# Optimization experiments

Hardware: AMD Instinct MI355X
Metric: run time of the kernel (lower is better)

The kernel has to match this reference:

```python
import jax, jax.numpy as jnp
import numpy as np

B, S, D = 2, 1024, 1024
H, KVH, HD = 16, 4, 64  # query heads, kv heads, head_dim
EPS = 1e-5
SCALE = float(np.sqrt(HD))  # note: scale uses original head_dim, not concat dim


def rmsnorm(x, g):
    return x * jax.lax.rsqrt(jnp.mean(x * x, axis=-1, keepdims=True) + EPS) * g


def rope(x, cos, sin):
    # x: [B,S,h,HD]; cos/sin: [S, HD//2]; pairs are consecutive (view_as_complex layout)
    xr = x.reshape(*x.shape[:-1], HD // 2, 2)
    x0, x1 = xr[..., 0], xr[..., 1]
    c = cos[None, :, None, :]
    s = sin[None, :, None, :]
    o0 = x0 * c - x1 * s
    o1 = x0 * s + x1 * c
    return jnp.stack([o0, o1], axis=-1).reshape(x.shape)


def context_build(x, W, gq, gk):
    comb = x @ W.T  # [B,S, H*HD + 2*KVH*HD]
    q, k, v = jnp.split(comb, [H * HD, H * HD + KVH * HD], axis=-1)
    q = rmsnorm(q, gq).reshape(B, S, H, HD)
    k = rmsnorm(k, gk).reshape(B, S, KVH, HD)
    v = v.reshape(B, S, KVH, HD)
    return q, k, v


def setup_inputs() -> dict:
    key = jax.random.key(0)
    ks = jax.random.split(key, 12)
    total = H * HD + 2 * KVH * HD  # 1536
    pos = jnp.arange(S, dtype=jnp.float32)
    theta = 10000.0 ** (-jnp.arange(0, HD, 2, dtype=jnp.float32) / HD)  # [HD//2]
    ang = pos[:, None] * theta[None, :]  # [S, HD//2]
    sc = 0.02
    return {
        "local_c": jax.random.normal(ks[0], (B, S, D), jnp.float32),
        "global_c": jax.random.normal(ks[1], (B, S, D), jnp.float32),
        "freqs_cos": jnp.cos(ang),
        "freqs_sin": jnp.sin(ang),
        "W_lc": jax.random.normal(ks[2], (total, D), jnp.float32) * sc,
        "W_gc": jax.random.normal(ks[3], (total, D), jnp.float32) * sc,
        "g_q_lc": jnp.ones((H * HD,), jnp.float32),
        "g_k_lc": jnp.ones((KVH * HD,), jnp.float32),
        "g_q_gc": jnp.ones((H * HD,), jnp.float32),
        "g_k_gc": jnp.ones((KVH * HD,), jnp.float32),
        "W_local": jax.random.normal(ks[4], (H * HD, 2 * H * HD), jnp.float32) * sc,
        "b_local": jnp.zeros((H * HD,), jnp.float32),
        "g_lc_out": jnp.ones((H * HD,), jnp.float32),
        "W_global": jax.random.normal(ks[5], (H * HD, 2 * H * HD), jnp.float32) * sc,
        "b_global": jnp.zeros((H * HD,), jnp.float32),
        "g_gc_out": jnp.ones((H * HD,), jnp.float32),
    }


def reference(local_c, global_c, freqs_cos, freqs_sin, W_lc, W_gc,
              g_q_lc, g_k_lc, g_q_gc, g_k_gc,
              W_local, b_local, g_lc_out, W_global, b_global, g_gc_out):
    q_lc, k_lc, v_lc = context_build(local_c, W_lc, g_q_lc, g_k_lc)
    q_gc, k_gc, v_gc = context_build(global_c, W_gc, g_q_gc, g_k_gc)

    q_lc = rope(q_lc, freqs_cos, freqs_sin)
    k_lc = rope(k_lc, freqs_cos, freqs_sin)
    q_gc = rope(q_gc, freqs_cos, freqs_sin)
    k_gc = rope(k_gc, freqs_cos, freqs_sin)

    # concat local+global along head_dim -> per-head dim 2*HD
    q = jnp.concatenate([q_lc, q_gc], axis=-1)  # [B,S,H,2HD]
    k = jnp.concatenate([k_lc, k_gc], axis=-1)  # [B,S,KVH,2HD]
    v = jnp.concatenate([v_lc, v_gc], axis=-1)

    n_rep = H // KVH
    k = jnp.repeat(k, n_rep, axis=2)  # [B,S,H,2HD] (GQA repeat_kv)
    v = jnp.repeat(v, n_rep, axis=2)

    scores = jnp.einsum("bqhd,bkhd->bhqk", q, k) / SCALE  # [B,H,S,S]
    attn = jax.nn.softmax(scores, axis=-1)
    out = jnp.einsum("bhqk,bkhd->bqhd", attn, v).reshape(B, S, H * 2 * HD)

    x_lc = rmsnorm(out @ W_local.T + b_local, g_lc_out)
    x_gc = rmsnorm(out @ W_global.T + b_global, g_gc_out)
    return (x_lc, x_gc)
```

## Files before the change

kernel.cpp:

```cpp
#include <hip/hip_runtime.h>

typedef __attribute__((ext_vector_type(8))) __bf16 bf16x8;
typedef __attribute__((ext_vector_type(4))) __bf16 bf16x4;
typedef __attribute__((ext_vector_type(4))) float f32x4;

__device__ __forceinline__ bf16x8 cvt8(const float* __restrict__ p)
{
    const float4 a = *(const float4*)p;
    const float4 b = *(const float4*)(p + 4);
    bf16x8 r;
    r[0] = (__bf16)a.x; r[1] = (__bf16)a.y; r[2] = (__bf16)a.z; r[3] = (__bf16)a.w;
    r[4] = (__bf16)b.x; r[5] = (__bf16)b.y; r[6] = (__bf16)b.z; r[7] = (__bf16)b.w;
    return r;
}

__device__ __forceinline__ void gld16(const __bf16* g, __bf16* l)
{
    __builtin_amdgcn_global_load_lds(
        (const __attribute__((address_space(1))) void*)g,
        (__attribute__((address_space(3))) void*)l, 16, 0, 0);
}

struct CvtArgs {
    const float* s[6];
    __bf16* d[6];
    int n[6];
};

__global__ __launch_bounds__(256) void cvt_bf16(CvtArgs a)
{
    const int t = blockIdx.y;
    const int i0 = (blockIdx.x * 256 + threadIdx.x) * 8;
    if (i0 < a.n[t])
        *(bf16x8*)(a.d[t] + i0) = cvt8(a.s[t] + i0);
}

template <typename CT>
__device__ __forceinline__ void gemm_core(const __bf16* __restrict__ Ap, int lda,
                                          const __bf16* __restrict__ Bp, int ldb,
                                          CT* __restrict__ Cp, int ldc, int K)
{
    __shared__ __bf16 As[2][128 * 32];
    __shared__ __bf16 Bs[2][128 * 32];
    const int tid  = threadIdx.x;
    const int w    = tid >> 6;
    const int lane = tid & 63;
    const int ln   = lane & 15;
    const int quad = lane >> 4;
    const int wm   = w & 1;
    const int wn   = w >> 1;

    const int srow = 32 * w + (lane >> 2);
    const int scol = (lane & 3) * 8;

    f32x4 acc[4][4];
    const f32x4 zero = {0.f, 0.f, 0.f, 0.f};
#pragma unroll
    for (int i = 0; i < 4; i++)
#pragma unroll
        for (int j = 0; j < 4; j++) acc[i][j] = zero;

    auto stage = [&](int buf, int k0) {
        gld16(Ap + (size_t)srow * lda        + k0 + scol, As[buf] + (2 * w)     * 512 + lane * 8);
        gld16(Ap + (size_t)(srow + 16) * lda + k0 + scol, As[buf] + (2 * w + 1) * 512 + lane * 8);
        gld16(Bp + (size_t)srow * ldb        + k0 + scol, Bs[buf] + (2 * w)     * 512 + lane * 8);
        gld16(Bp + (size_t)(srow + 16) * ldb + k0 + scol, Bs[buf] + (2 * w + 1) * 512 + lane * 8);
    };

    stage(0, 0);
    int buf = 0;
    for (int k0 = 0; k0 < K; k0 += 32, buf ^= 1) {
        __syncthreads();
        if (k0 + 32 < K) stage(buf ^ 1, k0 + 32);

        bf16x8 af[4], bw[4];
#pragma unroll
        for (int i = 0; i < 4; i++)
            af[i] = *(const bf16x8*)(As[buf] + (wm * 64 + i * 16 + ln) * 32 + quad * 8);
#pragma unroll
        for (int j = 0; j < 4; j++)
            bw[j] = *(const bf16x8*)(Bs[buf] + (wn * 64 + j * 16 + ln) * 32 + quad * 8);
#pragma unroll
        for (int i = 0; i < 4; i++)
#pragma unroll
            for (int j = 0; j < 4; j++)
                acc[i][j] = __builtin_amdgcn_mfma_f32_16x16x32_bf16(
                    af[i], bw[j], acc[i][j], 0, 0, 0);
    }

#pragma unroll
    for (int i = 0; i < 4; i++)
#pragma unroll
        for (int j = 0; j < 4; j++)
#pragma unroll
            for (int r = 0; r < 4; r++) {
                const int ml = wm * 64 + i * 16 + quad * 4 + r;
                const int nl = wn * 64 + j * 16 + ln;
                Cp[(size_t)ml * ldc + nl] = (CT)acc[i][j][r];
            }
}

__global__ __launch_bounds__(256) void gemm_qkv(const __bf16* __restrict__ Xbf,
                                                const __bf16* __restrict__ Wqkv,
                                                __bf16* __restrict__ comb)
{
    const int z = blockIdx.z;
    const __bf16* A = Xbf  + (size_t)z * 2048 * 1024 + (size_t)blockIdx.y * 128 * 1024;
    const __bf16* B = Wqkv + (size_t)z * 1536 * 1024 + (size_t)blockIdx.x * 128 * 1024;
    __bf16* C = comb + (size_t)z * 2048 * 1536 +
                (size_t)blockIdx.y * 128 * 1536 + (size_t)blockIdx.x * 128;
    gemm_core<__bf16>(A, 1024, B, 1024, C, 1536, 1024);
}

__global__ __launch_bounds__(256) void gemm_out(const __bf16* __restrict__ AO,
                                                const __bf16* __restrict__ Wout,
                                                __bf16* __restrict__ Y0,
                                                __bf16* __restrict__ Y1)
{
    const int kh = blockIdx.z;
    const __bf16* A = AO   + (size_t)blockIdx.y * 128 * 2048 + kh * 1024;
    const __bf16* B = Wout + (size_t)blockIdx.x * 128 * 2048 + kh * 1024;
    __bf16* Y = kh ? Y1 : Y0;
    __bf16* C = Y + (size_t)blockIdx.y * 128 * 2048 + (size_t)blockIdx.x * 128;
    gemm_core<__bf16>(A, 2048, B, 2048, C, 2048, 1024);
}

__global__ __launch_bounds__(256) void pack_qkv(
    const __bf16* __restrict__ comb,
    const float* __restrict__ fcos, const float* __restrict__ fsin,
    const float* __restrict__ g_q_lc, const float* __restrict__ g_k_lc,
    const float* __restrict__ g_q_gc, const float* __restrict__ g_k_gc,
    __bf16* __restrict__ Qb, __bf16* __restrict__ Kb, __bf16* __restrict__ Vb)
{
    const int m = blockIdx.x, ctx = blockIdx.y;
    const int b = m >> 10, s = m & 1023;
    const int tid = threadIdx.x;
    const __bf16* cr = comb + ((size_t)ctx * 2048 + m) * 1536;
    const float* gq = ctx ? g_q_gc : g_q_lc;
    const float* gk = ctx ? g_k_gc : g_k_lc;

    const bf16x4 qv = *(const bf16x4*)(cr + tid * 4);
    float sq = (float)qv[0] * (float)qv[0] + (float)qv[1] * (float)qv[1] +
               (float)qv[2] * (float)qv[2] + (float)qv[3] * (float)qv[3];
    const float kvv = (float)cr[1024 + tid];
    float sk = kvv * kvv;
#pragma unroll
    for (int off = 32; off > 0; off >>= 1) {
        sq += __shfl_down(sq, off);
        sk += __shfl_down(sk, off);
    }
    __shared__ float redq[4], redk[4];
    if ((tid & 63) == 0) { redq[tid >> 6] = sq; redk[tid >> 6] = sk; }
    __syncthreads();
    sq = redq[0] + redq[1] + redq[2] + redq[3];
    sk = redk[0] + redk[1] + redk[2] + redk[3];
    const float rq = rsqrtf(sq * (1.f / 1024.f) + 1e-5f);
    const float rk = rsqrtf(sk * (1.f / 256.f) + 1e-5f);

#pragma unroll
    for (int pp = 0; pp < 2; pp++) {
        const int p = tid + pp * 256;
        const int h = p >> 5, pi = p & 31;
        const float x0 = (float)cr[2 * p]     * rq * gq[2 * p];
        const float x1 = (float)cr[2 * p + 1] * rq * gq[2 * p + 1];
        const float c  = fcos[s * 32 + pi];
        const float sn = fsin[s * 32 + pi];
        const float o0 = (x0 * c - x1 * sn) * 0.125f;
        const float o1 = (x0 * sn + x1 * c) * 0.125f;
        const size_t qo = ((size_t)m * 16 + h) * 128 + ctx * 64 + 2 * pi;
        Qb[qo]     = (__bf16)o0;
        Qb[qo + 1] = (__bf16)o1;
    }
    if (tid < 128) {
        const int p = tid;
        const int kvh = p >> 5, pi = p & 31;
        const float x0 = (float)cr[1024 + 2 * p]     * rk * gk[2 * p];
        const float x1 = (float)cr[1024 + 2 * p + 1] * rk * gk[2 * p + 1];
        const float c  = fcos[s * 32 + pi];
        const float sn = fsin[s * 32 + pi];
        const float o0 = x0 * c - x1 * sn;
        const float o1 = x0 * sn + x1 * c;
        const size_t ko = ((size_t)(b * 4 + kvh) * 1024 + s) * 128 + ctx * 64 + 2 * pi;
        Kb[ko]     = (__bf16)o0;
        Kb[ko + 1] = (__bf16)o1;
    }
    {
        const int kvh = tid >> 6, d = tid & 63;
        Vb[((size_t)(b * 4 + kvh) * 1024 + s) * 128 + ctx * 64 + d] = cr[1280 + tid];
    }
}

__global__ __launch_bounds__(256) void v_transpose(const __bf16* __restrict__ Vb,
                                                   __bf16* __restrict__ Vtb)
{
    __shared__ __bf16 lds[64 * 64];
    const int st  = blockIdx.x;
    const int dt  = blockIdx.y;
    const int bkv = blockIdx.z;
    const int tid = threadIdx.x;
    const __bf16* src = Vb  + ((size_t)bkv * 1024 + st * 64) * 128 + dt * 64;
    __bf16*       dst = Vtb + ((size_t)bkv * 128 + dt * 64) * 1024 + st * 64;

#pragma unroll
    for (int i = 0; i < 2; i++) {
        const int c = tid + i * 256;
        const int s_in = c >> 3, ch = c & 7;
        const bf16x8 v = *(const bf16x8*)(src + (size_t)s_in * 128 + ch * 8);
        *(bf16x8*)&lds[s_in * 64 + (((ch + (s_in >> 3)) & 7) * 8)] = v;
    }
    __syncthreads();
#pragma unroll
    for (int i = 0; i < 2; i++) {
        const int c = tid + i * 256;
        const int dd = c >> 3, s0 = (c & 7) * 8;
        bf16x8 o;
#pragma unroll
        for (int jj = 0; jj < 8; jj++) {
            const int s = s0 + jj;
            o[jj] = lds[s * 64 + ((((dd >> 3) + (s >> 3)) & 7) * 8) + (dd & 7)];
        }
        *(bf16x8*)(dst + (size_t)dd * 1024 + s0) = o;
    }
}

__global__ __launch_bounds__(512) void attn(const __bf16* __restrict__ Qb,
                                            const __bf16* __restrict__ Kb,
                                            const __bf16* __restrict__ Vtb,
                                            __bf16* __restrict__ AO)
{
    __shared__ __bf16 Ks[2][64][136];
    __shared__ __bf16 Vts[2][128][72];
    __shared__ __bf16 Ps[4][16][72];
    __shared__ float Lsum[2][4][16];

    const int tid  = threadIdx.x;
    const int w    = tid >> 6;
    const int wq   = w >> 1;
    const int wk   = w & 1;
    const int lane = tid & 63;
    const int ln   = lane & 15;
    const int quad = lane >> 4;
    const int qt = blockIdx.x, h = blockIdx.y, b = blockIdx.z;
    const int kv = h >> 2;

    const __bf16* Kbase = Kb  + (size_t)(b * 4 + kv) * 1024 * 128;
    const __bf16* Vbase = Vtb + (size_t)(b * 4 + kv) * 128 * 1024;

    bf16x8 qf[4];
    const int qrow = qt * 64 + wq * 16 + ln;
    const __bf16* qptr = Qb + ((size_t)(b * 1024 + qrow) * 16 + h) * 128;
#pragma unroll
    for (int kc = 0; kc < 4; kc++)
        qf[kc] = *(const bf16x8*)(qptr + kc * 32 + quad * 8);

    f32x4 oacc[4];
    const f32x4 zero = {0.f, 0.f, 0.f, 0.f};
#pragma unroll
    for (int j = 0; j < 4; j++) oacc[j] = zero;
    float lpart[4] = {0.f, 0.f, 0.f, 0.f};

    bf16x8 kreg[2], vreg[2];
    auto load_tiles = [&](int kt) {
        const int ks0 = kt * 64;
#pragma unroll
        for (int i = 0; i < 2; i++) {
            const int c = tid + i * 512;
            kreg[i] = *(const bf16x8*)(Kbase + (size_t)(ks0 + (c >> 4)) * 128 + (c & 15) * 8);
            vreg[i] = *(const bf16x8*)(Vbase + (size_t)(c >> 3) * 1024 + ks0 + (c & 7) * 8);
        }
    };
    auto write_tiles = [&](int buf) {
#pragma unroll
        for (int i = 0; i < 2; i++) {
            const int c = tid + i * 512;
            *(bf16x8*)&Ks[buf][c >> 4][(c & 15) * 8] = kreg[i];
            *(bf16x8*)&Vts[buf][c >> 3][(c & 7) * 8] = vreg[i];
        }
    };

    load_tiles(0);
    write_tiles(0);

    for (int kt = 0; kt < 16; kt++) {
        const int buf = kt & 1;
        if (kt + 1 < 16) load_tiles(kt + 1);
        __syncthreads();

        f32x4 sacc[2];
#pragma unroll
        for (int j = 0; j < 2; j++) {
            f32x4 a = zero;
#pragma unroll
            for (int kc = 0; kc < 4; kc++) {
                const bf16x8 kf =
                    *(const bf16x8*)&Ks[buf][wk * 32 + j * 16 + ln][kc * 32 + quad * 8];
                a = __builtin_amdgcn_mfma_f32_16x16x32_bf16(qf[kc], kf, a, 0, 0, 0);
            }
            sacc[j] = a;
        }

#pragma unroll
        for (int j = 0; j < 2; j++)
#pragma unroll
            for (int r = 0; r < 4; r++) {
                const float p = __expf(sacc[j][r] - 20.f);
                lpart[r] += p;
                Ps[wq][quad * 4 + r][wk * 32 + j * 16 + ln] = (__bf16)p;
            }

        __syncthreads();

#pragma unroll
        for (int kk = 0; kk < 2; kk++) {
            const bf16x8 pf = *(const bf16x8*)&Ps[wq][ln][kk * 32 + quad * 8];
#pragma unroll
            for (int j2 = 0; j2 < 4; j2++) {
                const bf16x8 vf =
                    *(const bf16x8*)&Vts[buf][wk * 64 + j2 * 16 + ln][kk * 32 + quad * 8];
                oacc[j2] = __builtin_amdgcn_mfma_f32_16x16x32_bf16(pf, vf, oacc[j2], 0, 0, 0);
            }
        }

        if (kt + 1 < 16) write_tiles(buf ^ 1);
    }

    float lrow[4];
#pragma unroll
    for (int r = 0; r < 4; r++) {
        float rs = lpart[r];
#pragma unroll
        for (int off = 1; off < 16; off <<= 1)
            rs += __shfl_xor(rs, off);
        lrow[r] = rs;
    }
    __syncthreads();
    if (ln == 0) {
#pragma unroll
        for (int r = 0; r < 4; r++)
            Lsum[wk][wq][quad * 4 + r] = lrow[r];
    }
    __syncthreads();
    float inv[4];
#pragma unroll
    for (int r = 0; r < 4; r++)
        inv[r] = 1.f / (Lsum[0][wq][quad * 4 + r] + Lsum[1][wq][quad * 4 + r]);

#pragma unroll
    for (int j2 = 0; j2 < 4; j2++)
#pragma unroll
        for (int r = 0; r < 4; r++) {
            const size_t row = (size_t)(b * 1024 + qt * 64 + wq * 16 + quad * 4 + r);
            AO[row * 2048 + h * 128 + wk * 64 + j2 * 16 + ln] =
                (__bf16)(oacc[j2][r] * inv[r]);
        }
}

__global__ __launch_bounds__(256) void rmsnorm_out(const __bf16* __restrict__ Y0,
                                                   const __bf16* __restrict__ Y1,
                                                   const float* __restrict__ b_l,
                                                   const float* __restrict__ b_g,
                                                   const float* __restrict__ g_l,
                                                   const float* __restrict__ g_g,
                                                   float* __restrict__ out)
{
    const int m = blockIdx.x, which = blockIdx.y;
    const int tid = threadIdx.x;
    const size_t off = (size_t)m * 2048 + which * 1024 + tid * 4;
    const float* bias = which ? b_g : b_l;
    const float* g    = which ? g_g : g_l;

    const bf16x4 y0 = *(const bf16x4*)(Y0 + off);
    const bf16x4 y1 = *(const bf16x4*)(Y1 + off);
    const float4 bv = *(const float4*)(bias + tid * 4);
    float x[4];
    x[0] = (float)y0[0] + (float)y1[0] + bv.x;
    x[1] = (float)y0[1] + (float)y1[1] + bv.y;
    x[2] = (float)y0[2] + (float)y1[2] + bv.z;
    x[3] = (float)y0[3] + (float)y1[3] + bv.w;
    float ss = x[0] * x[0] + x[1] * x[1] + x[2] * x[2] + x[3] * x[3];
#pragma unroll
    for (int off2 = 32; off2 > 0; off2 >>= 1) ss += __shfl_down(ss, off2);
    __shared__ float red[4];
    if ((tid & 63) == 0) red[tid >> 6] = ss;
    __syncthreads();
    ss = red[0] + red[1] + red[2] + red[3];
    const float r = rsqrtf(ss * (1.f / 1024.f) + 1e-5f);

    const float4 gv = *(const float4*)(g + tid * 4);
    float4 o;
    o.x = x[0] * r * gv.x;
    o.y = x[1] * r * gv.y;
    o.z = x[2] * r * gv.z;
    o.w = x[3] * r * gv.w;
    *(float4*)(out + (size_t)which * 2097152 + (size_t)m * 1024 + tid * 4) = o;
}

extern "C" void kernel_launch(void* const* d_in, const int* in_sizes, int n_in,
                              void* d_out, int out_size, void* d_ws, size_t ws_size,
                              hipStream_t stream)
{
    (void)in_sizes; (void)n_in; (void)out_size; (void)ws_size;
    const float* local_c  = (const float*)d_in[0];
    const float* global_c = (const float*)d_in[1];
    const float* fcos     = (const float*)d_in[2];
    const float* fsin     = (const float*)d_in[3];
    const float* W_lc     = (const float*)d_in[4];
    const float* W_gc     = (const float*)d_in[5];
    const float* g_q_lc   = (const float*)d_in[6];
    const float* g_k_lc   = (const float*)d_in[7];
    const float* g_q_gc   = (const float*)d_in[8];
    const float* g_k_gc   = (const float*)d_in[9];
    const float* W_local  = (const float*)d_in[10];
    const float* b_local  = (const float*)d_in[11];
    const float* g_lc_out = (const float*)d_in[12];
    const float* W_global = (const float*)d_in[13];
    const float* b_global = (const float*)d_in[14];
    const float* g_gc_out = (const float*)d_in[15];

    char* ws = (char*)d_ws;
    __bf16* Wout = (__bf16*)(ws + 0);
    __bf16* Xbf  = (__bf16*)(ws + 8388608);
    __bf16* Wqkv = (__bf16*)(ws + 16777216);
    __bf16* comb = (__bf16*)(ws + 23068672);
    __bf16* Qb   = (__bf16*)(ws + 35651584);
    __bf16* Kb   = (__bf16*)(ws + 44040192);
    __bf16* Vtb  = (__bf16*)(ws + 46137344);
    __bf16* AO   = (__bf16*)(ws + 48234496);
    __bf16* Y0   = (__bf16*)(ws + 56623104);
    __bf16* Y1   = (__bf16*)(ws + 65011712);
    __bf16* Vb   = (__bf16*)(ws + 56623104);

    CvtArgs ca;
    ca.s[0] = local_c;  ca.d[0] = Xbf;            ca.n[0] = 2097152;
    ca.s[1] = global_c; ca.d[1] = Xbf + 2097152;  ca.n[1] = 2097152;
    ca.s[2] = W_lc;     ca.d[2] = Wqkv;           ca.n[2] = 1572864;
    ca.s[3] = W_gc;     ca.d[3] = Wqkv + 1572864; ca.n[3] = 1572864;
    ca.s[4] = W_local;  ca.d[4] = Wout;           ca.n[4] = 2097152;
    ca.s[5] = W_global; ca.d[5] = Wout + 2097152; ca.n[5] = 2097152;

    cvt_bf16<<<dim3(1024, 6), 256, 0, stream>>>(ca);
    gemm_qkv<<<dim3(12, 16, 2), 256, 0, stream>>>(Xbf, Wqkv, comb);
    pack_qkv<<<dim3(2048, 2), 256, 0, stream>>>(comb, fcos, fsin,
                                                g_q_lc, g_k_lc, g_q_gc, g_k_gc,
                                                Qb, Kb, Vb);
    v_transpose<<<dim3(16, 2, 8), 256, 0, stream>>>(Vb, Vtb);
    attn<<<dim3(16, 16, 2), 512, 0, stream>>>(Qb, Kb, Vtb, AO);
    gemm_out<<<dim3(16, 16, 2), 256, 0, stream>>>(AO, Wout, Y0, Y1);
    rmsnorm_out<<<dim3(2048, 2), 256, 0, stream>>>(Y0, Y1, b_local, b_global,
                                                   g_lc_out, g_gc_out,
                                                   (float*)d_out);
}
```

Before: 213.1 us.

## Split attention PV across waves by key to drop the mid-loop barrier

```diff
diff --git a/kernel.cpp b/kernel.cpp
--- a/kernel.cpp
+++ b/kernel.cpp
@@ -223,14 +223,14 @@
     }
 }
 
-__global__ __launch_bounds__(512) void attn(const __bf16* __restrict__ Qb,
-                                            const __bf16* __restrict__ Kb,
-                                            const __bf16* __restrict__ Vtb,
-                                            __bf16* __restrict__ AO)
-{
-    __shared__ __bf16 Ks[2][64][136];
-    __shared__ __bf16 Vts[2][128][72];
-    __shared__ __bf16 Ps[4][16][72];
+__global__ __launch_bounds__(512, 4) void attn(const __bf16* __restrict__ Qb,
+                                               const __bf16* __restrict__ Kb,
+                                               const __bf16* __restrict__ Vtb,
+                                               __bf16* __restrict__ AO)
+{
+    __shared__ __align__(16) __bf16 Ks[2][64][132];
+    __shared__ __align__(16) __bf16 Vts[2][128][72];
+    __shared__ __align__(16) __bf16 Ps[8][16][36];
     __shared__ float Lsum[2][4][16];
 
     const int tid  = threadIdx.x;
@@ -247,16 +247,18 @@
     const __bf16* Vbase = Vtb + (size_t)(b * 4 + kv) * 128 * 1024;
 
     bf16x8 qf[4];
-    const int qrow = qt * 64 + wq * 16 + ln;
-    const __bf16* qptr = Qb + ((size_t)(b * 1024 + qrow) * 16 + h) * 128;
-#pragma unroll
-    for (int kc = 0; kc < 4; kc++)
-        qf[kc] = *(const bf16x8*)(qptr + kc * 32 + quad * 8);
-
-    f32x4 oacc[4];
+    {
+        const int qrow = qt * 64 + wq * 16 + ln;
+        const __bf16* qptr = Qb + ((size_t)(b * 1024 + qrow) * 16 + h) * 128;
+#pragma unroll
+        for (int kc = 0; kc < 4; kc++)
+            qf[kc] = *(const bf16x8*)(qptr + kc * 32 + quad * 8);
+    }
+
+    f32x4 oacc[8];
     const f32x4 zero = {0.f, 0.f, 0.f, 0.f};
 #pragma unroll
-    for (int j = 0; j < 4; j++) oacc[j] = zero;
+    for (int j = 0; j < 8; j++) oacc[j] = zero;
     float lpart[4] = {0.f, 0.f, 0.f, 0.f};
 
     bf16x8 kreg[2], vreg[2];
@@ -284,9 +286,11 @@
     for (int kt = 0; kt < 16; kt++) {
         const int buf = kt & 1;
         if (kt + 1 < 16) load_tiles(kt + 1);
-        __syncthreads();
+
+        asm volatile("s_waitcnt lgkmcnt(0)\n\ts_barrier" ::: "memory");
 
         f32x4 sacc[2];
+        __builtin_amdgcn_s_setprio(1);
 #pragma unroll
         for (int j = 0; j < 2; j++) {
             f32x4 a = zero;
@@ -298,6 +302,7 @@
             }
             sacc[j] = a;
         }
+        __builtin_amdgcn_s_setprio(0);
 
 #pragma unroll
         for (int j = 0; j < 2; j++)
@@ -305,21 +310,18 @@
             for (int r = 0; r < 4; r++) {
                 const float p = __expf(sacc[j][r] - 20.f);
                 lpart[r] += p;
-                Ps[wq][quad * 4 + r][wk * 32 + j * 16 + ln] = (__bf16)p;
+                Ps[w][quad * 4 + r][j * 16 + ln] = (__bf16)p;
             }
 
-        __syncthreads();
-
-#pragma unroll
-        for (int kk = 0; kk < 2; kk++) {
-            const bf16x8 pf = *(const bf16x8*)&Ps[wq][ln][kk * 32 + quad * 8];
-#pragma unroll
-            for (int j2 = 0; j2 < 4; j2++) {
-                const bf16x8 vf =
-                    *(const bf16x8*)&Vts[buf][wk * 64 + j2 * 16 + ln][kk * 32 + quad * 8];
-                oacc[j2] = __builtin_amdgcn_mfma_f32_16x16x32_bf16(pf, vf, oacc[j2], 0, 0, 0);
-            }
+        const bf16x8 pf = *(const bf16x8*)&Ps[w][ln][quad * 8];
+        __builtin_amdgcn_s_setprio(1);
+#pragma unroll
+        for (int j2 = 0; j2 < 8; j2++) {
+            const bf16x8 vf =
+                *(const bf16x8*)&Vts[buf][j2 * 16 + ln][wk * 32 + quad * 8];
+            oacc[j2] = __builtin_amdgcn_mfma_f32_16x16x32_bf16(pf, vf, oacc[j2], 0, 0, 0);
         }
+        __builtin_amdgcn_s_setprio(0);
 
         if (kt + 1 < 16) write_tiles(buf ^ 1);
     }
@@ -333,26 +335,37 @@
             rs += __shfl_xor(rs, off);
         lrow[r] = rs;
     }
-    __syncthreads();
     if (ln == 0) {
 #pragma unroll
         for (int r = 0; r < 4; r++)
             Lsum[wk][wq][quad * 4 + r] = lrow[r];
     }
     __syncthreads();
-    float inv[4];
-#pragma unroll
-    for (int r = 0; r < 4; r++)
-        inv[r] = 1.f / (Lsum[0][wq][quad * 4 + r] + Lsum[1][wq][quad * 4 + r]);
-
-#pragma unroll
-    for (int j2 = 0; j2 < 4; j2++)
-#pragma unroll
-        for (int r = 0; r < 4; r++) {
-            const size_t row = (size_t)(b * 1024 + qt * 64 + wq * 16 + quad * 4 + r);
-            AO[row * 2048 + h * 128 + wk * 64 + j2 * 16 + ln] =
-                (__bf16)(oacc[j2][r] * inv[r]);
-        }
+
+    float* scr = (float*)&Vts[0][0][0];
+    if (wk == 1) {
+#pragma unroll
+        for (int j2 = 0; j2 < 8; j2++)
+#pragma unroll
+            for (int r = 0; r < 4; r++)
+                scr[(wq * 16 + quad * 4 + r) * 132 + j2 * 16 + ln] = oacc[j2][r];
+    }
+    __syncthreads();
+    if (wk == 0) {
+        float inv[4];
+#pragma unroll
+        for (int r = 0; r < 4; r++)
+            inv[r] = 1.f / (Lsum[0][wq][quad * 4 + r] + Lsum[1][wq][quad * 4 + r]);
+#pragma unroll
+        for (int j2 = 0; j2 < 8; j2++)
+#pragma unroll
+            for (int r = 0; r < 4; r++) {
+                const float v = oacc[j2][r] +
+                    scr[(wq * 16 + quad * 4 + r) * 132 + j2 * 16 + ln];
+                const size_t row = (size_t)(b * 1024 + qt * 64 + wq * 16 + quad * 4 + r);
+                AO[row * 2048 + h * 128 + j2 * 16 + ln] = (__bf16)(v * inv[r]);
+            }
+    }
 }
 
 __global__ __launch_bounds__(256) void rmsnorm_out(const __bf16* __restrict__ Y0,
```

Result: no change. 212.5 us (-0.3%).
